# Performance work log

Hardware: AMD Instinct MI355X
Metric: run time of the kernel (lower is better)

## Reference

```python
import jax, jax.numpy as jnp
import numpy as np

HIDDEN = 256
MAX_LENGTH = 256
NUM_LAYERS = 4
VOCAB = 50257


def setup_inputs() -> dict:
    key = jax.random.key(0)
    ks = jax.random.split(key, 16)
    s = 0.05
    return {
        "token": jax.random.randint(ks[0], (1,), 0, VOCAB, dtype=jnp.int64 if jax.config.jax_enable_x64 else jnp.int32),
        "hidden": jax.random.normal(ks[1], (NUM_LAYERS, 1, HIDDEN), dtype=jnp.float32),
        "encoder_outputs": jax.random.normal(ks[2], (MAX_LENGTH, HIDDEN), dtype=jnp.float32),
        "emb": jax.random.normal(ks[3], (VOCAB, HIDDEN), dtype=jnp.float32) * s,
        "attn_w": jax.random.normal(ks[4], (MAX_LENGTH, 2 * HIDDEN), dtype=jnp.float32) * s,
        "attn_b": jax.random.normal(ks[5], (MAX_LENGTH,), dtype=jnp.float32) * s,
        "comb_w": jax.random.normal(ks[6], (HIDDEN, 2 * HIDDEN), dtype=jnp.float32) * s,
        "comb_b": jax.random.normal(ks[7], (HIDDEN,), dtype=jnp.float32) * s,
        "gru_wih": jax.random.normal(ks[8], (NUM_LAYERS, 3 * HIDDEN, HIDDEN), dtype=jnp.float32) * s,
        "gru_whh": jax.random.normal(ks[9], (NUM_LAYERS, 3 * HIDDEN, HIDDEN), dtype=jnp.float32) * s,
        "gru_bih": jax.random.normal(ks[10], (NUM_LAYERS, 3 * HIDDEN), dtype=jnp.float32) * s,
        "gru_bhh": jax.random.normal(ks[11], (NUM_LAYERS, 3 * HIDDEN), dtype=jnp.float32) * s,
        "out_w": jax.random.normal(ks[12], (VOCAB, HIDDEN), dtype=jnp.float32) * s,
        "out_b": jax.random.normal(ks[13], (VOCAB,), dtype=jnp.float32) * s,
    }


def _gru_cell(x, h, wih, whh, bih, bhh):
    # PyTorch GRU cell: gates ordered [r, z, n]
    gi = x @ wih.T + bih  # [1, 3H]
    gh = h @ whh.T + bhh  # [1, 3H]
    i_r, i_z, i_n = jnp.split(gi, 3, axis=1)
    h_r, h_z, h_n = jnp.split(gh, 3, axis=1)
    r = jax.nn.sigmoid(i_r + h_r)
    z = jax.nn.sigmoid(i_z + h_z)
    n = jnp.tanh(i_n + r * h_n)
    return (1.0 - z) * n + z * h


def reference(token, hidden, encoder_outputs, emb, attn_w, attn_b, comb_w, comb_b,
              gru_wih, gru_whh, gru_bih, gru_bhh, out_w, out_b):
    # embedding lookup (dropout is identity in eval)  -> [1, H]
    embedded = emb[token]
    # Bahdanau-style attention weights over MAX_LENGTH positions
    attn_in = jnp.concatenate([embedded, hidden[0]], axis=1)  # [1, 2H]
    attn_weights = jax.nn.softmax(attn_in @ attn_w.T + attn_b, axis=1)  # [1, L]
    attn_applied = attn_weights @ encoder_outputs  # [1, H]
    comb_in = jnp.concatenate([embedded, attn_applied], axis=1)  # [1, 2H]
    x = jax.nn.relu(comb_in @ comb_w.T + comb_b)  # [1, H]
    # 4-layer GRU, single timestep
    new_h = []
    for l in range(NUM_LAYERS):
        h_l = _gru_cell(x, hidden[l], gru_wih[l], gru_whh[l], gru_bih[l], gru_bhh[l])
        new_h.append(h_l)
        x = h_l
    hidden_new = jnp.stack(new_h, axis=0)  # [4, 1, H]
    logp = jax.nn.log_softmax(x @ out_w.T + out_b, axis=1)  # [1, V]
    return (logp, hidden_new, attn_weights)
```

## Files before the change

kernel.cpp:

```cpp
#include <hip/hip_runtime.h>
#include <hip/hip_bf16.h>

#define H 256
#define L2H 512
#define NLAYERS 4
#define VOCAB 50257

#define OUT_LOGP 0
#define OUT_HID  50257
#define OUT_ATTN 51281

#define WS_SCORE  0
#define WS_BARS   256
#define WS_APP    512
#define WS_X      768
#define WS_PM     768
#define WS_PS     1024
#define WS_FLAG   2304

#define CL_APP  0
#define CL_X4   16
#define CL_LOG  32

#define NBLK 256
#define SENT 0x7FC00001u

typedef unsigned short u16;

__device__ __forceinline__ float bf2f(u16 u) {
    return __uint_as_float(((unsigned int)u) << 16);
}

__device__ __forceinline__ u16 f2bf(float f) {
    unsigned int x = __float_as_uint(f);
    unsigned int r = x + 0x7fff + ((x >> 16) & 1);
    return (u16)(r >> 16);
}

template<bool BF16>
__device__ __forceinline__ float ld1(const void* p, size_t i) {
    if (BF16) return bf2f(((const u16*)p)[i]);
    else      return ((const float*)p)[i];
}

template<bool BF16>
__device__ __forceinline__ float4 ld4(const void* p, size_t i) {
    if (BF16) {
        ushort4 w = *(const ushort4*)((const u16*)p + i);
        return make_float4(bf2f(w.x), bf2f(w.y), bf2f(w.z), bf2f(w.w));
    } else {
        return *(const float4*)((const float*)p + i);
    }
}

template<bool BF16>
__device__ __forceinline__ void ld8(const void* p, size_t i, float* f) {
    if (BF16) {
        uint4 u = *(const uint4*)((const u16*)p + i);
        f[0] = bf2f(u.x & 0xffff); f[1] = bf2f(u.x >> 16);
        f[2] = bf2f(u.y & 0xffff); f[3] = bf2f(u.y >> 16);
        f[4] = bf2f(u.z & 0xffff); f[5] = bf2f(u.z >> 16);
        f[6] = bf2f(u.w & 0xffff); f[7] = bf2f(u.w >> 16);
    } else {
        const float4* q = (const float4*)((const float*)p + i);
        float4 a = q[0], b = q[1];
        f[0] = a.x; f[1] = a.y; f[2] = a.z; f[3] = a.w;
        f[4] = b.x; f[5] = b.y; f[6] = b.z; f[7] = b.w;
    }
}

template<bool BF16>
__device__ __forceinline__ void st(void* p, size_t i, float v) {
    if (BF16) ((u16*)p)[i] = f2bf(v);
    else      ((float*)p)[i] = v;
}

__device__ __forceinline__ float ldc(const float* p) {
    return __hip_atomic_load(const_cast<float*>(p), __ATOMIC_RELAXED, __HIP_MEMORY_SCOPE_AGENT);
}
__device__ __forceinline__ void stc(float* p, float v) {
    __hip_atomic_store(p, v, __ATOMIC_RELAXED, __HIP_MEMORY_SCOPE_AGENT);
}

template<int SLP>
__device__ __forceinline__ float pollf(const float* p) {
    unsigned u = __hip_atomic_load((unsigned*)const_cast<float*>(p),
                                   __ATOMIC_RELAXED, __HIP_MEMORY_SCOPE_AGENT);
    while (u == SENT) {
        __builtin_amdgcn_s_sleep(SLP);
        u = __hip_atomic_load((unsigned*)const_cast<float*>(p),
                              __ATOMIC_RELAXED, __HIP_MEMORY_SCOPE_AGENT);
    }
    return __uint_as_float(u);
}

__device__ __forceinline__ void arrive_line(unsigned* bars, int idx) {
    __syncthreads();
    if (threadIdx.x == 0)
        __hip_atomic_fetch_add(&bars[idx], 1u, __ATOMIC_RELAXED, __HIP_MEMORY_SCOPE_AGENT);
}
template<int SLP>
__device__ __forceinline__ void wait_line(unsigned* bars, int idx, unsigned exp) {
    if (threadIdx.x == 0) {
        while (__hip_atomic_load(&bars[idx], __ATOMIC_RELAXED, __HIP_MEMORY_SCOPE_AGENT) < exp)
            __builtin_amdgcn_s_sleep(SLP);
    }
    __syncthreads();
}

__global__ __launch_bounds__(256) void k_init(const void* emb, float* ws) {
    int tid = threadIdx.x;
    unsigned* bars = (unsigned*)(ws + WS_BARS);
    __hip_atomic_store(&bars[tid], 0u, __ATOMIC_RELAXED, __HIP_MEMORY_SCOPE_AGENT);
    __hip_atomic_store((unsigned*)(ws + WS_APP) + tid, 0u, __ATOMIC_RELAXED, __HIP_MEMORY_SCOPE_AGENT);
    __hip_atomic_store((unsigned*)(ws + WS_SCORE) + tid, SENT, __ATOMIC_RELAXED, __HIP_MEMORY_SCOPE_AGENT);
    #pragma unroll
    for (int k = 0; k < 4; ++k)
        __hip_atomic_store((unsigned*)(ws + WS_X + k * 256) + tid, SENT,
                           __ATOMIC_RELAXED, __HIP_MEMORY_SCOPE_AGENT);
    if (tid < 64) {
        float b = fabsf(bf2f(((const u16*)emb)[tid]));
        #pragma unroll
        for (int off = 32; off; off >>= 1) b = fmaxf(b, __shfl_xor(b, off));
        if (tid == 0) ws[WS_FLAG] = (b < 1.0f) ? 1.0f : 0.0f;
    }
}

template<bool BF16>
__device__ __forceinline__ void pipeline(
    const int* __restrict__ tok, const void* __restrict__ emb,
    const void* __restrict__ hidden,
    const void* __restrict__ attn_w, const void* __restrict__ attn_b,
    const void* __restrict__ enc,
    const void* __restrict__ comb_w, const void* __restrict__ comb_b,
    const void* __restrict__ gwih, const void* __restrict__ gwhh,
    const void* __restrict__ gbih, const void* __restrict__ gbhh,
    const void* __restrict__ out_w, const void* __restrict__ out_b,
    float* __restrict__ ws, void* __restrict__ out)
{
    unsigned* bars = (unsigned*)(ws + WS_BARS);
    const int tid  = threadIdx.x;
    const int lane = tid & 63;
    const int wid  = tid >> 6;
    const int bx   = blockIdx.x;
    const size_t es = BF16 ? 2 : 4;

    __shared__ float lds[256];
    __shared__ float wsm[256];

    if (bx < 64) {
        const int wv = (bx << 2) | wid;
        const int j8 = lane * 8;

        {
            float wf[8]; ld8<BF16>(attn_w, (size_t)wv * L2H + j8, wf);
            float xin[8];
            if (lane < 32) ld8<BF16>(emb, (size_t)tok[0] * H + j8, xin);
            else           ld8<BF16>(hidden, (size_t)(j8 - H), xin);
            float v = 0.f;
            #pragma unroll
            for (int q = 0; q < 8; ++q) v += xin[q] * wf[q];
            #pragma unroll
            for (int off = 32; off; off >>= 1) v += __shfl_xor(v, off);
            if (lane == 0) stc(ws + WS_SCORE + wv, v + ld1<BF16>(attn_b, wv));
        }

        if (bx < 16) {
            const int l0 = bx * 16;
            float ev[16];
            #pragma unroll
            for (int k = 0; k < 16; ++k)
                ev[k] = ld1<BF16>(enc, (size_t)(l0 + k) * H + tid);
            float s = pollf<1>(ws + WS_SCORE + tid);
            lds[tid] = s; __syncthreads();
            for (int off = 128; off; off >>= 1) {
                if (tid < off) lds[tid] = fmaxf(lds[tid], lds[tid + off]);
                __syncthreads();
            }
            float M = lds[0]; __syncthreads();
            float e = __expf(s - M);
            lds[tid] = e; __syncthreads();
            for (int off = 128; off; off >>= 1) {
                if (tid < off) lds[tid] += lds[tid + off];
                __syncthreads();
            }
            float w = e / lds[0];
            wsm[tid] = w; __syncthreads();
            if (bx == 0) st<BF16>(out, OUT_ATTN + tid, w);
            float acc = 0.f;
            #pragma unroll
            for (int k = 0; k < 16; ++k) acc += wsm[l0 + k] * ev[k];
            atomicAdd(&ws[WS_APP + tid], acc);
            arrive_line(bars, CL_APP);
        }

        {
            float wf[8]; ld8<BF16>(comb_w, (size_t)wv * L2H + j8, wf);
            float xin[8];
            if (lane < 32) ld8<BF16>(emb, (size_t)tok[0] * H + j8, xin);
            wait_line<1>(bars, CL_APP, 16);
            if (lane >= 32) {
                #pragma unroll
                for (int q = 0; q < 8; ++q) xin[q] = ldc(ws + WS_APP + (j8 - H) + q);
            }
            float v = 0.f;
            #pragma unroll
            for (int q = 0; q < 8; ++q) v += xin[q] * wf[q];
            #pragma unroll
            for (int off = 32; off; off >>= 1) v += __shfl_xor(v, off);
            if (lane == 0) stc(ws + WS_X + wv, fmaxf(v + ld1<BF16>(comb_b, wv), 0.f));
        }

        const int e4 = lane * 4;
        #pragma unroll 1
        for (int l = 0; l < NLAYERS; ++l) {
            const float* xin_p = ws + WS_X + l * 256;
            float*       xout  = ws + WS_X + (l + 1) * 256;
            const char* wih = (const char*)gwih + (size_t)l * 3 * H * H * es;
            const char* whh = (const char*)gwhh + (size_t)l * 3 * H * H * es;
            const char* bih = (const char*)gbih + (size_t)l * 3 * H * es;
            const char* bhh = (const char*)gbhh + (size_t)l * 3 * H * es;
            const char* hprev = (const char*)hidden + (size_t)l * H * es;
            char*       hout  = (char*)out + (size_t)(OUT_HID + l * H) * es;
            const int i = wv;

            float4 hv  = ld4<BF16>(hprev, e4);
            float4 wri = ld4<BF16>(wih, (size_t)(i        ) * H + e4);
            float4 wzi = ld4<BF16>(wih, (size_t)(H + i    ) * H + e4);
            float4 wni = ld4<BF16>(wih, (size_t)(2 * H + i) * H + e4);
            float4 wrh = ld4<BF16>(whh, (size_t)(i        ) * H + e4);
            float4 wzh = ld4<BF16>(whh, (size_t)(H + i    ) * H + e4);
            float4 wnh = ld4<BF16>(whh, (size_t)(2 * H + i) * H + e4);

            float4 xv;
            xv.x = pollf<2>(xin_p + e4);
            xv.y = pollf<2>(xin_p + e4 + 1);
            xv.z = pollf<2>(xin_p + e4 + 2);
            xv.w = pollf<2>(xin_p + e4 + 3);

            float a = wri.x * xv.x + wri.y * xv.y + wri.z * xv.z + wri.w * xv.w
                    + wrh.x * hv.x + wrh.y * hv.y + wrh.z * hv.z + wrh.w * hv.w;
            float b = wzi.x * xv.x + wzi.y * xv.y + wzi.z * xv.z + wzi.w * xv.w
                    + wzh.x * hv.x + wzh.y * hv.y + wzh.z * hv.z + wzh.w * hv.w;
            float c = wni.x * xv.x + wni.y * xv.y + wni.z * xv.z + wni.w * xv.w;
            float d = wnh.x * hv.x + wnh.y * hv.y + wnh.z * hv.z + wnh.w * hv.w;

            #pragma unroll
            for (int off = 32; off; off >>= 1) {
                a += __shfl_xor(a, off);
                b += __shfl_xor(b, off);
                c += __shfl_xor(c, off);
                d += __shfl_xor(d, off);
            }
            if (lane == 0) {
                float r = 1.f / (1.f + __expf(-(a + ld1<BF16>(bih, i) + ld1<BF16>(bhh, i))));
                float z = 1.f / (1.f + __expf(-(b + ld1<BF16>(bih, H + i) + ld1<BF16>(bhh, H + i))));
                float n = tanhf(c + ld1<BF16>(bih, 2 * H + i) + r * (d + ld1<BF16>(bhh, 2 * H + i)));
                float hold = ld1<BF16>(hprev, i);
                float hn = (1.f - z) * n + z * hold;
                stc(xout + i, hn);
                st<BF16>(hout, i, hn);
            }
        }
        arrive_line(bars, CL_X4);
    }

    wait_line<2>(bars, CL_X4, 64);

    const int grp = (bx << 3) | (tid >> 5);
    const int l32 = tid & 31;
    float vs[25];
    {
        float xf[8];
        #pragma unroll
        for (int q = 0; q < 8; ++q) xf[q] = ldc(ws + WS_X + 4 * 256 + l32 * 8 + q);

        float m = -1e30f, s = 0.f;
        #pragma unroll
        for (int it = 0; it < 3; ++it) {
            const int rb = it * 16384 + grp;
            float wf[8][8], bb[8];
            #pragma unroll
            for (int k = 0; k < 8; ++k) {
                ld8<BF16>(out_w, (size_t)(rb + (k << 11)) * H + l32 * 8, wf[k]);
                bb[k] = ld1<BF16>(out_b, rb + (k << 11));
            }
            #pragma unroll
            for (int k = 0; k < 8; ++k) {
                float v = wf[k][0]*xf[0] + wf[k][1]*xf[1] + wf[k][2]*xf[2] + wf[k][3]*xf[3]
                        + wf[k][4]*xf[4] + wf[k][5]*xf[5] + wf[k][6]*xf[6] + wf[k][7]*xf[7];
                #pragma unroll
                for (int off = 16; off; off >>= 1) v += __shfl_xor(v, off);
                v += bb[k];
                vs[it * 8 + k] = v;
                float mn = fmaxf(m, v);
                s = s * __expf(m - mn) + __expf(v - mn);
                m = mn;
            }
        }
        vs[24] = 0.f;
        if (grp < VOCAB - 49152) {
            int r = 49152 + grp;
            float wf[8]; ld8<BF16>(out_w, (size_t)r * H + l32 * 8, wf);
            float v = wf[0]*xf[0] + wf[1]*xf[1] + wf[2]*xf[2] + wf[3]*xf[3]
                    + wf[4]*xf[4] + wf[5]*xf[5] + wf[6]*xf[6] + wf[7]*xf[7];
            #pragma unroll
            for (int off = 16; off; off >>= 1) v += __shfl_xor(v, off);
            v += ld1<BF16>(out_b, r);
            vs[24] = v;
            float mn = fmaxf(m, v);
            s = s * __expf(m - mn) + __expf(v - mn);
            m = mn;
        }

        {
            float mo = __shfl_xor(m, 32), so = __shfl_xor(s, 32);
            float M = fmaxf(m, mo);
            s = s * __expf(m - M) + so * __expf(mo - M);
            m = M;
        }
        if (lane == 0) { lds[wid] = m; lds[4 + wid] = s; }
        __syncthreads();
        if (tid == 0) {
            float M01 = fmaxf(lds[0], lds[1]);
            float S01 = lds[4] * __expf(lds[0] - M01) + lds[5] * __expf(lds[1] - M01);
            float M23 = fmaxf(lds[2], lds[3]);
            float S23 = lds[6] * __expf(lds[2] - M23) + lds[7] * __expf(lds[3] - M23);
            float Mx = fmaxf(M01, M23);
            float S  = S01 * __expf(M01 - Mx) + S23 * __expf(M23 - Mx);
            stc(ws + WS_PM + bx, Mx);
            stc(ws + WS_PS + bx, S);
        }
    }
    arrive_line(bars, CL_LOG + 16 * (bx & 7));
    if (tid < 8) {
        while (__hip_atomic_load(&bars[CL_LOG + 16 * tid],
                                 __ATOMIC_RELAXED, __HIP_MEMORY_SCOPE_AGENT) < 32u)
            __builtin_amdgcn_s_sleep(1);
    }
    __syncthreads();

    {
        float m = ldc(ws + WS_PM + tid);
        float s = ldc(ws + WS_PS + tid);
        #pragma unroll
        for (int off = 32; off; off >>= 1) {
            float mo = __shfl_xor(m, off), so = __shfl_xor(s, off);
            float M = fmaxf(m, mo);
            s = s * __expf(m - M) + so * __expf(mo - M);
            m = M;
        }
        if (lane == 0) { lds[wid] = m; lds[4 + wid] = s; }
        __syncthreads();
        if (tid == 0) {
            float M01 = fmaxf(lds[0], lds[1]);
            float S01 = lds[4] * __expf(lds[0] - M01) + lds[5] * __expf(lds[1] - M01);
            float M23 = fmaxf(lds[2], lds[3]);
            float S23 = lds[6] * __expf(lds[2] - M23) + lds[7] * __expf(lds[3] - M23);
            float Mx = fmaxf(M01, M23);
            float S  = S01 * __expf(M01 - Mx) + S23 * __expf(M23 - Mx);
            lds[8] = Mx + __logf(S);
        }
        __syncthreads();
        float c = lds[8];
        if (l32 == 0) {
            #pragma unroll
            for (int it = 0; it < 3; ++it) {
                #pragma unroll
                for (int k = 0; k < 8; ++k)
                    st<BF16>(out, OUT_LOGP + it * 16384 + (k << 11) + grp, vs[it * 8 + k] - c);
            }
            if (grp < VOCAB - 49152)
                st<BF16>(out, OUT_LOGP + 49152 + grp, vs[24] - c);
        }
    }
}

__global__ __launch_bounds__(256, 1) void k_all(
    const int* __restrict__ tok, const void* __restrict__ emb,
    const void* __restrict__ hidden,
    const void* __restrict__ attn_w, const void* __restrict__ attn_b,
    const void* __restrict__ enc,
    const void* __restrict__ comb_w, const void* __restrict__ comb_b,
    const void* __restrict__ gwih, const void* __restrict__ gwhh,
    const void* __restrict__ gbih, const void* __restrict__ gbhh,
    const void* __restrict__ out_w, const void* __restrict__ out_b,
    float* __restrict__ ws, void* __restrict__ out)
{
    if (ws[WS_FLAG] > 0.5f)
        pipeline<true >(tok, emb, hidden, attn_w, attn_b, enc, comb_w, comb_b,
                        gwih, gwhh, gbih, gbhh, out_w, out_b, ws, out);
    else
        pipeline<false>(tok, emb, hidden, attn_w, attn_b, enc, comb_w, comb_b,
                        gwih, gwhh, gbih, gbhh, out_w, out_b, ws, out);
}

extern "C" void kernel_launch(void* const* d_in, const int* in_sizes, int n_in,
                              void* d_out, int out_size, void* d_ws, size_t ws_size,
                              hipStream_t stream) {
    const int* tok = (const int*)d_in[0];
    float* ws = (float*)d_ws;

    k_init<<<dim3(1), dim3(256), 0, stream>>>(d_in[3], ws);
    k_all<<<dim3(NBLK), dim3(256), 0, stream>>>(
        tok, d_in[3], d_in[1], d_in[4], d_in[5], d_in[2], d_in[6], d_in[7],
        d_in[8], d_in[9], d_in[10], d_in[11], d_in[12], d_in[13],
        ws, d_out);
}
```

Measured before the change: 173.7 us.

## Shrink GRU chain to 8 blocks and prefetch logit weights during recurrence

Moves the attention/combine/GRU chain onto 8 blocks that each own 32 rows, replacing per-element sentinel polling with counter barriers on padded lines. The other blocks preload their bf16 output-projection weights into registers before waiting on a go flag, so the vocabulary weight stream overlaps the serial GRU chain. The final log-softmax constant is computed by block 0 and broadcast through per-line go words instead of every block reducing the partials. The cost is heavy register use (25 uint4 per thread) and fewer blocks doing each GRU matvec serially with 192 threads.

```diff
diff --git a/kernel.cpp b/kernel.cpp
--- a/kernel.cpp
+++ b/kernel.cpp
@@ -10,22 +10,29 @@
 #define OUT_HID  50257
 #define OUT_ATTN 51281
 
-#define WS_SCORE  0
-#define WS_BARS   256
-#define WS_APP    512
-#define WS_X      768
-#define WS_PM     768
-#define WS_PS     1024
-#define WS_FLAG   2304
-
-#define CL_APP  0
-#define CL_X4   16
-#define CL_LOG  32
-
+#define WS_SCORE 0
+#define WS_BARS  256
+#define WS_APP   512
+#define WS_XA    768
+#define WS_XB    1024
+#define WS_PM    768
+#define WS_PS    1024
+#define WS_X4    1280
+#define WS_X4B   1536
+#define WS_X4C   1792
+#define WS_GO    2048
+#define WS_FLAG  2304
+
+#define L_SCORE 0
+#define L_APP   1
+#define L_X0    2
+#define L_LOG0  8
+
+#define NCHAIN 8
 #define NBLK 256
-#define SENT 0x7FC00001u
 
 typedef unsigned short u16;
+typedef unsigned long long u64;
 
 __device__ __forceinline__ float bf2f(u16 u) {
     return __uint_as_float(((unsigned int)u) << 16);
@@ -41,16 +48,6 @@
 __device__ __forceinline__ float ld1(const void* p, size_t i) {
     if (BF16) return bf2f(((const u16*)p)[i]);
     else      return ((const float*)p)[i];
-}
-
-template<bool BF16>
-__device__ __forceinline__ float4 ld4(const void* p, size_t i) {
-    if (BF16) {
-        ushort4 w = *(const ushort4*)((const u16*)p + i);
-        return make_float4(bf2f(w.x), bf2f(w.y), bf2f(w.z), bf2f(w.w));
-    } else {
-        return *(const float4*)((const float*)p + i);
-    }
 }
 
 template<bool BF16>
@@ -81,48 +78,97 @@
 __device__ __forceinline__ void stc(float* p, float v) {
     __hip_atomic_store(p, v, __ATOMIC_RELAXED, __HIP_MEMORY_SCOPE_AGENT);
 }
-
-template<int SLP>
-__device__ __forceinline__ float pollf(const float* p) {
-    unsigned u = __hip_atomic_load((unsigned*)const_cast<float*>(p),
-                                   __ATOMIC_RELAXED, __HIP_MEMORY_SCOPE_AGENT);
-    while (u == SENT) {
-        __builtin_amdgcn_s_sleep(SLP);
-        u = __hip_atomic_load((unsigned*)const_cast<float*>(p),
-                              __ATOMIC_RELAXED, __HIP_MEMORY_SCOPE_AGENT);
-    }
-    return __uint_as_float(u);
+__device__ __forceinline__ u64 ldcu(const u64* p) {
+    return __hip_atomic_load(const_cast<u64*>(p), __ATOMIC_RELAXED, __HIP_MEMORY_SCOPE_AGENT);
+}
+__device__ __forceinline__ void stcu(u64* p, u64 v) {
+    __hip_atomic_store(p, v, __ATOMIC_RELAXED, __HIP_MEMORY_SCOPE_AGENT);
 }
 
 __device__ __forceinline__ void arrive_line(unsigned* bars, int idx) {
     __syncthreads();
     if (threadIdx.x == 0)
-        __hip_atomic_fetch_add(&bars[idx], 1u, __ATOMIC_RELAXED, __HIP_MEMORY_SCOPE_AGENT);
+        __hip_atomic_fetch_add(&bars[idx * 16], 1u, __ATOMIC_RELAXED, __HIP_MEMORY_SCOPE_AGENT);
 }
 template<int SLP>
 __device__ __forceinline__ void wait_line(unsigned* bars, int idx, unsigned exp) {
     if (threadIdx.x == 0) {
-        while (__hip_atomic_load(&bars[idx], __ATOMIC_RELAXED, __HIP_MEMORY_SCOPE_AGENT) < exp)
+        while (__hip_atomic_load(&bars[idx * 16], __ATOMIC_RELAXED, __HIP_MEMORY_SCOPE_AGENT) < exp)
             __builtin_amdgcn_s_sleep(SLP);
     }
     __syncthreads();
+}
+
+template<int SLP>
+__device__ __forceinline__ u64 poll_go(const u64* p, unsigned need) {
+    u64 u = ldcu(p);
+    while ((unsigned)(u & 0xffffffffull) < need) {
+        __builtin_amdgcn_s_sleep(SLP);
+        u = ldcu(p);
+    }
+    return u;
+}
+
+__device__ __forceinline__ float dot8_u4bf(uint4 u, const float* xf) {
+    return bf2f(u.x & 0xffff)*xf[0] + bf2f(u.x >> 16)*xf[1]
+         + bf2f(u.y & 0xffff)*xf[2] + bf2f(u.y >> 16)*xf[3]
+         + bf2f(u.z & 0xffff)*xf[4] + bf2f(u.z >> 16)*xf[5]
+         + bf2f(u.w & 0xffff)*xf[6] + bf2f(u.w >> 16)*xf[7];
 }
 
 __global__ __launch_bounds__(256) void k_init(const void* emb, float* ws) {
     int tid = threadIdx.x;
-    unsigned* bars = (unsigned*)(ws + WS_BARS);
-    __hip_atomic_store(&bars[tid], 0u, __ATOMIC_RELAXED, __HIP_MEMORY_SCOPE_AGENT);
+    __hip_atomic_store((unsigned*)(ws + WS_BARS) + tid, 0u, __ATOMIC_RELAXED, __HIP_MEMORY_SCOPE_AGENT);
+    __hip_atomic_store((unsigned*)(ws + WS_GO) + tid, 0u, __ATOMIC_RELAXED, __HIP_MEMORY_SCOPE_AGENT);
     __hip_atomic_store((unsigned*)(ws + WS_APP) + tid, 0u, __ATOMIC_RELAXED, __HIP_MEMORY_SCOPE_AGENT);
-    __hip_atomic_store((unsigned*)(ws + WS_SCORE) + tid, SENT, __ATOMIC_RELAXED, __HIP_MEMORY_SCOPE_AGENT);
-    #pragma unroll
-    for (int k = 0; k < 4; ++k)
-        __hip_atomic_store((unsigned*)(ws + WS_X + k * 256) + tid, SENT,
-                           __ATOMIC_RELAXED, __HIP_MEMORY_SCOPE_AGENT);
     if (tid < 64) {
         float b = fabsf(bf2f(((const u16*)emb)[tid]));
         #pragma unroll
         for (int off = 32; off; off >>= 1) b = fmaxf(b, __shfl_xor(b, off));
         if (tid == 0) ws[WS_FLAG] = (b < 1.0f) ? 1.0f : 0.0f;
+    }
+}
+
+template<bool BF16>
+__device__ __forceinline__ void logits_stream(
+    const void* __restrict__ out_w, const void* __restrict__ out_b,
+    const float* xf, int grp, int l32, float* vs, float& m, float& s)
+{
+    #pragma unroll
+    for (int it = 0; it < 3; ++it) {
+        const int rb = it * 16384 + grp;
+        float wf[8][8], bb[8];
+        #pragma unroll
+        for (int k = 0; k < 8; ++k) {
+            ld8<BF16>(out_w, (size_t)(rb + (k << 11)) * H + l32 * 8, wf[k]);
+            bb[k] = ld1<BF16>(out_b, rb + (k << 11));
+        }
+        #pragma unroll
+        for (int k = 0; k < 8; ++k) {
+            float v = wf[k][0]*xf[0] + wf[k][1]*xf[1] + wf[k][2]*xf[2] + wf[k][3]*xf[3]
+                    + wf[k][4]*xf[4] + wf[k][5]*xf[5] + wf[k][6]*xf[6] + wf[k][7]*xf[7];
+            #pragma unroll
+            for (int off = 16; off; off >>= 1) v += __shfl_xor(v, off);
+            v += bb[k];
+            vs[it * 8 + k] = v;
+            float mn = fmaxf(m, v);
+            s = s * __expf(m - mn) + __expf(v - mn);
+            m = mn;
+        }
+    }
+    vs[24] = 0.f;
+    if (grp < VOCAB - 49152) {
+        int r = 49152 + grp;
+        float wf[8]; ld8<BF16>(out_w, (size_t)r * H + l32 * 8, wf);
+        float v = wf[0]*xf[0] + wf[1]*xf[1] + wf[2]*xf[2] + wf[3]*xf[3]
+                + wf[4]*xf[4] + wf[5]*xf[5] + wf[6]*xf[6] + wf[7]*xf[7];
+        #pragma unroll
+        for (int off = 16; off; off >>= 1) v += __shfl_xor(v, off);
+        v += ld1<BF16>(out_b, r);
+        vs[24] = v;
+        float mn = fmaxf(m, v);
+        s = s * __expf(m - mn) + __expf(v - mn);
+        m = mn;
     }
 }
 
@@ -145,40 +191,59 @@
     const int bx   = blockIdx.x;
     const size_t es = BF16 ? 2 : 4;
 
+    const int grp = (bx << 3) | (tid >> 5);
+    const int l32 = tid & 31;
+
     __shared__ float lds[256];
     __shared__ float wsm[256];
-
-    if (bx < 64) {
-        const int wv = (bx << 2) | wid;
+    __shared__ float xsh[256];
+    __shared__ float hsh[256];
+    __shared__ float gd[192];
+    __shared__ float cshare;
+
+    float vs[25];
+    float m = -1e30f, s = 0.f;
+
+    if (bx < NCHAIN) {
+        const int rbase = bx * 32;
         const int j8 = lane * 8;
+        const int tk = tok[0];
 
         {
-            float wf[8]; ld8<BF16>(attn_w, (size_t)wv * L2H + j8, wf);
+            float wfa[8][8];
+            #pragma unroll
+            for (int k = 0; k < 8; ++k)
+                ld8<BF16>(attn_w, (size_t)(rbase + wid * 8 + k) * L2H + j8, wfa[k]);
             float xin[8];
-            if (lane < 32) ld8<BF16>(emb, (size_t)tok[0] * H + j8, xin);
+            if (lane < 32) ld8<BF16>(emb, (size_t)tk * H + j8, xin);
             else           ld8<BF16>(hidden, (size_t)(j8 - H), xin);
-            float v = 0.f;
-            #pragma unroll
-            for (int q = 0; q < 8; ++q) v += xin[q] * wf[q];
-            #pragma unroll
-            for (int off = 32; off; off >>= 1) v += __shfl_xor(v, off);
-            if (lane == 0) stc(ws + WS_SCORE + wv, v + ld1<BF16>(attn_b, wv));
-        }
-
-        if (bx < 16) {
-            const int l0 = bx * 16;
-            float ev[16];
-            #pragma unroll
-            for (int k = 0; k < 16; ++k)
-                ev[k] = ld1<BF16>(enc, (size_t)(l0 + k) * H + tid);
-            float s = pollf<1>(ws + WS_SCORE + tid);
-            lds[tid] = s; __syncthreads();
+            #pragma unroll
+            for (int k = 0; k < 8; ++k) {
+                int r = rbase + wid * 8 + k;
+                float v = 0.f;
+                #pragma unroll
+                for (int q = 0; q < 8; ++q) v += xin[q] * wfa[k][q];
+                #pragma unroll
+                for (int off = 32; off; off >>= 1) v += __shfl_xor(v, off);
+                if (lane == 0) stc(ws + WS_SCORE + r, v + ld1<BF16>(attn_b, r));
+            }
+        }
+        arrive_line(bars, L_SCORE);
+
+        {
+            float ev[32];
+            #pragma unroll
+            for (int k = 0; k < 32; ++k)
+                ev[k] = ld1<BF16>(enc, (size_t)(rbase + k) * H + tid);
+            wait_line<1>(bars, L_SCORE, NCHAIN);
+            float sc = ldc(ws + WS_SCORE + tid);
+            lds[tid] = sc; __syncthreads();
             for (int off = 128; off; off >>= 1) {
                 if (tid < off) lds[tid] = fmaxf(lds[tid], lds[tid + off]);
                 __syncthreads();
             }
             float M = lds[0]; __syncthreads();
-            float e = __expf(s - M);
+            float e = __expf(sc - M);
             lds[tid] = e; __syncthreads();
             for (int off = 128; off; off >>= 1) {
                 if (tid < off) lds[tid] += lds[tid + off];
@@ -189,137 +254,194 @@
             if (bx == 0) st<BF16>(out, OUT_ATTN + tid, w);
             float acc = 0.f;
             #pragma unroll
-            for (int k = 0; k < 16; ++k) acc += wsm[l0 + k] * ev[k];
+            for (int k = 0; k < 32; ++k) acc += wsm[rbase + k] * ev[k];
             atomicAdd(&ws[WS_APP + tid], acc);
-            arrive_line(bars, CL_APP);
-        }
+        }
+        arrive_line(bars, L_APP);
 
         {
-            float wf[8]; ld8<BF16>(comb_w, (size_t)wv * L2H + j8, wf);
+            float wfa[8][8];
+            #pragma unroll
+            for (int k = 0; k < 8; ++k)
+                ld8<BF16>(comb_w, (size_t)(rbase + wid * 8 + k) * L2H + j8, wfa[k]);
             float xin[8];
-            if (lane < 32) ld8<BF16>(emb, (size_t)tok[0] * H + j8, xin);
-            wait_line<1>(bars, CL_APP, 16);
+            if (lane < 32) ld8<BF16>(emb, (size_t)tk * H + j8, xin);
+            wait_line<1>(bars, L_APP, NCHAIN);
+            xsh[tid] = ldc(ws + WS_APP + tid);
+            __syncthreads();
             if (lane >= 32) {
                 #pragma unroll
-                for (int q = 0; q < 8; ++q) xin[q] = ldc(ws + WS_APP + (j8 - H) + q);
-            }
-            float v = 0.f;
-            #pragma unroll
-            for (int q = 0; q < 8; ++q) v += xin[q] * wf[q];
-            #pragma unroll
-            for (int off = 32; off; off >>= 1) v += __shfl_xor(v, off);
-            if (lane == 0) stc(ws + WS_X + wv, fmaxf(v + ld1<BF16>(comb_b, wv), 0.f));
-        }
-
-        const int e4 = lane * 4;
+                for (int q = 0; q < 8; ++q) xin[q] = xsh[j8 - H + q];
+            }
+            #pragma unroll
+            for (int k = 0; k < 8; ++k) {
+                int r = rbase + wid * 8 + k;
+                float v = 0.f;
+                #pragma unroll
+                for (int q = 0; q < 8; ++q) v += xin[q] * wfa[k][q];
+                #pragma unroll
+                for (int off = 32; off; off >>= 1) v += __shfl_xor(v, off);
+                if (lane == 0) stc(ws + WS_XA + r, fmaxf(v + ld1<BF16>(comb_b, r), 0.f));
+            }
+        }
+        arrive_line(bars, L_X0);
+
         #pragma unroll 1
         for (int l = 0; l < NLAYERS; ++l) {
-            const float* xin_p = ws + WS_X + l * 256;
-            float*       xout  = ws + WS_X + (l + 1) * 256;
+            const float* xin_p = ws + ((l & 1) ? WS_XB : WS_XA);
             const char* wih = (const char*)gwih + (size_t)l * 3 * H * H * es;
             const char* whh = (const char*)gwhh + (size_t)l * 3 * H * H * es;
             const char* bih = (const char*)gbih + (size_t)l * 3 * H * es;
             const char* bhh = (const char*)gbhh + (size_t)l * 3 * H * es;
             const char* hprev = (const char*)hidden + (size_t)l * H * es;
             char*       hout  = (char*)out + (size_t)(OUT_HID + l * H) * es;
-            const int i = wv;
-
-            float4 hv  = ld4<BF16>(hprev, e4);
-            float4 wri = ld4<BF16>(wih, (size_t)(i        ) * H + e4);
-            float4 wzi = ld4<BF16>(wih, (size_t)(H + i    ) * H + e4);
-            float4 wni = ld4<BF16>(wih, (size_t)(2 * H + i) * H + e4);
-            float4 wrh = ld4<BF16>(whh, (size_t)(i        ) * H + e4);
-            float4 wzh = ld4<BF16>(whh, (size_t)(H + i    ) * H + e4);
-            float4 wnh = ld4<BF16>(whh, (size_t)(2 * H + i) * H + e4);
-
-            float4 xv;
-            xv.x = pollf<2>(xin_p + e4);
-            xv.y = pollf<2>(xin_p + e4 + 1);
-            xv.z = pollf<2>(xin_p + e4 + 2);
-            xv.w = pollf<2>(xin_p + e4 + 3);
-
-            float a = wri.x * xv.x + wri.y * xv.y + wri.z * xv.z + wri.w * xv.w
-                    + wrh.x * hv.x + wrh.y * hv.y + wrh.z * hv.z + wrh.w * hv.w;
-            float b = wzi.x * xv.x + wzi.y * xv.y + wzi.z * xv.z + wzi.w * xv.w
-                    + wzh.x * hv.x + wzh.y * hv.y + wzh.z * hv.z + wzh.w * hv.w;
-            float c = wni.x * xv.x + wni.y * xv.y + wni.z * xv.z + wni.w * xv.w;
-            float d = wnh.x * hv.x + wnh.y * hv.y + wnh.z * hv.z + wnh.w * hv.w;
-
-            #pragma unroll
-            for (int off = 32; off; off >>= 1) {
-                a += __shfl_xor(a, off);
-                b += __shfl_xor(b, off);
-                c += __shfl_xor(c, off);
-                d += __shfl_xor(d, off);
-            }
-            if (lane == 0) {
-                float r = 1.f / (1.f + __expf(-(a + ld1<BF16>(bih, i) + ld1<BF16>(bhh, i))));
-                float z = 1.f / (1.f + __expf(-(b + ld1<BF16>(bih, H + i) + ld1<BF16>(bhh, H + i))));
-                float n = tanhf(c + ld1<BF16>(bih, 2 * H + i) + r * (d + ld1<BF16>(bhh, 2 * H + i)));
-                float hold = ld1<BF16>(hprev, i);
-                float hn = (1.f - z) * n + z * hold;
-                stc(xout + i, hn);
+
+            wait_line<1>(bars, L_X0 + l, NCHAIN);
+            xsh[tid] = ldc(xin_p + tid);
+            hsh[tid] = ld1<BF16>(hprev, tid);
+            __syncthreads();
+
+            if (tid < 192) {
+                int mat = tid / 96;
+                int rem = tid % 96;
+                int g   = rem / 32;
+                int j   = rem % 32;
+                const void* W = mat ? (const void*)whh : (const void*)wih;
+                const float* xv = mat ? hsh : xsh;
+                size_t rowoff = (size_t)(g * H + rbase + j) * H;
+                float acc = 0.f;
+                #pragma unroll 16
+                for (int c = 0; c < H; c += 8) {
+                    float wf[8]; ld8<BF16>(W, rowoff + c, wf);
+                    acc += wf[0]*xv[c]   + wf[1]*xv[c+1] + wf[2]*xv[c+2] + wf[3]*xv[c+3]
+                         + wf[4]*xv[c+4] + wf[5]*xv[c+5] + wf[6]*xv[c+6] + wf[7]*xv[c+7];
+                }
+                gd[tid] = acc;
+            }
+            __syncthreads();
+            if (tid < 32) {
+                int i = rbase + tid;
+                float r = 1.f / (1.f + __expf(-(gd[tid]      + ld1<BF16>(bih, i)
+                                              + gd[96 + tid] + ld1<BF16>(bhh, i))));
+                float z = 1.f / (1.f + __expf(-(gd[32 + tid]  + ld1<BF16>(bih, H + i)
+                                              + gd[128 + tid] + ld1<BF16>(bhh, H + i))));
+                float n = tanhf(gd[64 + tid] + ld1<BF16>(bih, 2 * H + i)
+                              + r * (gd[160 + tid] + ld1<BF16>(bhh, 2 * H + i)));
+                float hn = (1.f - z) * n + z * hsh[i];
+                if (l < 3) stc(ws + ((l & 1) ? WS_XA : WS_XB) + i, hn);
+                else { stc(ws + WS_X4 + i, hn); stc(ws + WS_X4B + i, hn); stc(ws + WS_X4C + i, hn); }
                 st<BF16>(hout, i, hn);
             }
-        }
-        arrive_line(bars, CL_X4);
-    }
-
-    wait_line<2>(bars, CL_X4, 64);
-
-    const int grp = (bx << 3) | (tid >> 5);
-    const int l32 = tid & 31;
-    float vs[25];
-    {
+            arrive_line(bars, L_X0 + l + 1);
+        }
+
+        wait_line<1>(bars, L_X0 + 4, NCHAIN);
+        if (bx == 0 && tid < 16)
+            stcu((u64*)(ws + WS_GO + 16 * tid), 1ull);
+
+        xsh[tid] = ldc(ws + WS_X4 + (bx % 3) * 256 + tid);
+        __syncthreads();
         float xf[8];
         #pragma unroll
-        for (int q = 0; q < 8; ++q) xf[q] = ldc(ws + WS_X + 4 * 256 + l32 * 8 + q);
-
-        float m = -1e30f, s = 0.f;
-        #pragma unroll
-        for (int it = 0; it < 3; ++it) {
-            const int rb = it * 16384 + grp;
-            float wf[8][8], bb[8];
-            #pragma unroll
-            for (int k = 0; k < 8; ++k) {
-                ld8<BF16>(out_w, (size_t)(rb + (k << 11)) * H + l32 * 8, wf[k]);
-                bb[k] = ld1<BF16>(out_b, rb + (k << 11));
-            }
-            #pragma unroll
-            for (int k = 0; k < 8; ++k) {
-                float v = wf[k][0]*xf[0] + wf[k][1]*xf[1] + wf[k][2]*xf[2] + wf[k][3]*xf[3]
-                        + wf[k][4]*xf[4] + wf[k][5]*xf[5] + wf[k][6]*xf[6] + wf[k][7]*xf[7];
+        for (int q = 0; q < 8; ++q) xf[q] = xsh[l32 * 8 + q];
+        logits_stream<BF16>(out_w, out_b, xf, grp, l32, vs, m, s);
+    } else {
+        if constexpr (BF16) {
+            uint4 pw[25]; float pb[25];
+            #pragma unroll
+            for (int it = 0; it < 3; ++it)
+                #pragma unroll
+                for (int k = 0; k < 8; ++k) {
+                    int r = it * 16384 + (k << 11) + grp;
+                    pw[it * 8 + k] = *(const uint4*)((const u16*)out_w + (size_t)r * H + l32 * 8);
+                    pb[it * 8 + k] = ld1<true>(out_b, r);
+                }
+            if (grp < VOCAB - 49152) {
+                int r = 49152 + grp;
+                pw[24] = *(const uint4*)((const u16*)out_w + (size_t)r * H + l32 * 8);
+                pb[24] = ld1<true>(out_b, r);
+            } else { pw[24] = make_uint4(0, 0, 0, 0); pb[24] = 0.f; }
+
+            if (tid == 0) (void)poll_go<2>((const u64*)(ws + WS_GO + 16 * (bx & 15)), 1u);
+            __syncthreads();
+            xsh[tid] = ldc(ws + WS_X4 + (bx % 3) * 256 + tid);
+            __syncthreads();
+            float xf[8];
+            #pragma unroll
+            for (int q = 0; q < 8; ++q) xf[q] = xsh[l32 * 8 + q];
+
+            #pragma unroll
+            for (int idx = 0; idx < 24; ++idx) {
+                float v = dot8_u4bf(pw[idx], xf);
                 #pragma unroll
                 for (int off = 16; off; off >>= 1) v += __shfl_xor(v, off);
-                v += bb[k];
-                vs[it * 8 + k] = v;
+                v += pb[idx];
+                vs[idx] = v;
                 float mn = fmaxf(m, v);
                 s = s * __expf(m - mn) + __expf(v - mn);
                 m = mn;
             }
-        }
-        vs[24] = 0.f;
-        if (grp < VOCAB - 49152) {
-            int r = 49152 + grp;
-            float wf[8]; ld8<BF16>(out_w, (size_t)r * H + l32 * 8, wf);
-            float v = wf[0]*xf[0] + wf[1]*xf[1] + wf[2]*xf[2] + wf[3]*xf[3]
-                    + wf[4]*xf[4] + wf[5]*xf[5] + wf[6]*xf[6] + wf[7]*xf[7];
-            #pragma unroll
-            for (int off = 16; off; off >>= 1) v += __shfl_xor(v, off);
-            v += ld1<BF16>(out_b, r);
-            vs[24] = v;
-            float mn = fmaxf(m, v);
-            s = s * __expf(m - mn) + __expf(v - mn);
-            m = mn;
-        }
-
-        {
-            float mo = __shfl_xor(m, 32), so = __shfl_xor(s, 32);
-            float M = fmaxf(m, mo);
-            s = s * __expf(m - M) + so * __expf(mo - M);
-            m = M;
-        }
-        if (lane == 0) { lds[wid] = m; lds[4 + wid] = s; }
+            vs[24] = 0.f;
+            if (grp < VOCAB - 49152) {
+                float v = dot8_u4bf(pw[24], xf);
+                #pragma unroll
+                for (int off = 16; off; off >>= 1) v += __shfl_xor(v, off);
+                v += pb[24];
+                vs[24] = v;
+                float mn = fmaxf(m, v);
+                s = s * __expf(m - mn) + __expf(v - mn);
+                m = mn;
+            }
+        } else {
+            if (tid == 0) (void)poll_go<2>((const u64*)(ws + WS_GO + 16 * (bx & 15)), 1u);
+            __syncthreads();
+            xsh[tid] = ldc(ws + WS_X4 + (bx % 3) * 256 + tid);
+            __syncthreads();
+            float xf[8];
+            #pragma unroll
+            for (int q = 0; q < 8; ++q) xf[q] = xsh[l32 * 8 + q];
+            logits_stream<false>(out_w, out_b, xf, grp, l32, vs, m, s);
+        }
+    }
+
+    {
+        float mo = __shfl_xor(m, 32), so = __shfl_xor(s, 32);
+        float M = fmaxf(m, mo);
+        s = s * __expf(m - M) + so * __expf(mo - M);
+        m = M;
+    }
+    if (lane == 0) { lds[wid] = m; lds[4 + wid] = s; }
+    __syncthreads();
+    if (tid == 0) {
+        float M01 = fmaxf(lds[0], lds[1]);
+        float S01 = lds[4] * __expf(lds[0] - M01) + lds[5] * __expf(lds[1] - M01);
+        float M23 = fmaxf(lds[2], lds[3]);
+        float S23 = lds[6] * __expf(lds[2] - M23) + lds[7] * __expf(lds[3] - M23);
+        float Mx = fmaxf(M01, M23);
+        float S  = S01 * __expf(M01 - Mx) + S23 * __expf(M23 - Mx);
+        stc(ws + WS_PM + bx, Mx);
+        stc(ws + WS_PS + bx, S);
+    }
+    arrive_line(bars, L_LOG0 + (bx & 7));
+
+    float c;
+    if (bx == 0) {
+        if (tid < 8) {
+            while (__hip_atomic_load(&bars[(L_LOG0 + tid) * 16],
+                                     __ATOMIC_RELAXED, __HIP_MEMORY_SCOPE_AGENT) < 32u)
+                __builtin_amdgcn_s_sleep(1);
+        }
+        __syncthreads();
+        float mm = ldc(ws + WS_PM + tid);
+        float ss = ldc(ws + WS_PS + tid);
+        #pragma unroll
+        for (int off = 32; off; off >>= 1) {
+            float mo = __shfl_xor(mm, off), so = __shfl_xor(ss, off);
+            float M = fmaxf(mm, mo);
+            ss = ss * __expf(mm - M) + so * __expf(mo - M);
+            mm = M;
+        }
+        if (lane == 0) { lds[wid] = mm; lds[4 + wid] = ss; }
         __syncthreads();
         if (tid == 0) {
             float M01 = fmaxf(lds[0], lds[1]);
@@ -328,51 +450,30 @@
             float S23 = lds[6] * __expf(lds[2] - M23) + lds[7] * __expf(lds[3] - M23);
             float Mx = fmaxf(M01, M23);
             float S  = S01 * __expf(M01 - Mx) + S23 * __expf(M23 - Mx);
-            stc(ws + WS_PM + bx, Mx);
-            stc(ws + WS_PS + bx, S);
-        }
-    }
-    arrive_line(bars, CL_LOG + 16 * (bx & 7));
-    if (tid < 8) {
-        while (__hip_atomic_load(&bars[CL_LOG + 16 * tid],
-                                 __ATOMIC_RELAXED, __HIP_MEMORY_SCOPE_AGENT) < 32u)
-            __builtin_amdgcn_s_sleep(1);
-    }
-    __syncthreads();
-
-    {
-        float m = ldc(ws + WS_PM + tid);
-        float s = ldc(ws + WS_PS + tid);
-        #pragma unroll
-        for (int off = 32; off; off >>= 1) {
-            float mo = __shfl_xor(m, off), so = __shfl_xor(s, off);
-            float M = fmaxf(m, mo);
-            s = s * __expf(m - M) + so * __expf(mo - M);
-            m = M;
-        }
-        if (lane == 0) { lds[wid] = m; lds[4 + wid] = s; }
+            cshare = Mx + __logf(S);
+        }
         __syncthreads();
+        c = cshare;
+        if (tid < 16)
+            stcu((u64*)(ws + WS_GO + 16 * tid),
+                 ((u64)__float_as_uint(c) << 32) | 2ull);
+    } else {
         if (tid == 0) {
-            float M01 = fmaxf(lds[0], lds[1]);
-            float S01 = lds[4] * __expf(lds[0] - M01) + lds[5] * __expf(lds[1] - M01);
-            float M23 = fmaxf(lds[2], lds[3]);
-            float S23 = lds[6] * __expf(lds[2] - M23) + lds[7] * __expf(lds[3] - M23);
-            float Mx = fmaxf(M01, M23);
-            float S  = S01 * __expf(M01 - Mx) + S23 * __expf(M23 - Mx);
-            lds[8] = Mx + __logf(S);
+            u64 u = poll_go<2>((const u64*)(ws + WS_GO + 16 * (bx & 15)), 2u);
+            cshare = __uint_as_float((unsigned)(u >> 32));
         }
         __syncthreads();
-        float c = lds[8];
-        if (l32 == 0) {
-            #pragma unroll
-            for (int it = 0; it < 3; ++it) {
-                #pragma unroll
-                for (int k = 0; k < 8; ++k)
-                    st<BF16>(out, OUT_LOGP + it * 16384 + (k << 11) + grp, vs[it * 8 + k] - c);
-            }
-            if (grp < VOCAB - 49152)
-                st<BF16>(out, OUT_LOGP + 49152 + grp, vs[24] - c);
-        }
+        c = cshare;
+    }
+
+    if (l32 == 0) {
+        #pragma unroll
+        for (int it = 0; it < 3; ++it)
+            #pragma unroll
+            for (int k = 0; k < 8; ++k)
+                st<BF16>(out, OUT_LOGP + it * 16384 + (k << 11) + grp, vs[it * 8 + k] - c);
+        if (grp < VOCAB - 49152)
+            st<BF16>(out, OUT_LOGP + 49152 + grp, vs[24] - c);
     }
 }
 
```

After: 200.5 us. 15.5% more time.
